# Optimization experiments

Hardware: AMD Instinct MI355X
Metric: run time of the kernel (lower is better)

The kernel has to match this reference:

```python
import jax, jax.numpy as jnp
import numpy as np

N_TOKENS, MODEL_DIM, NUM_EXPERTS = 65536, 1024, 64
CAPACITY_FACTOR = 1.0


def setup_inputs() -> dict:
    key = jax.random.key(0)
    k1, k2 = jax.random.split(key)
    x = jax.random.normal(k1, (N_TOKENS, MODEL_DIM), dtype=jnp.float32)
    # gate projection weight, torch Linear stores [out_features, in_features]
    wg = jax.random.normal(k2, (NUM_EXPERTS, MODEL_DIM), dtype=jnp.float32) * (1.0 / np.sqrt(MODEL_DIM))
    return {"x": x, "wg": wg}


def reference(x, wg):
    N, E = x.shape[0], wg.shape[0]
    logits = x @ wg.T                              # [N, E]
    # training-branch capacity: capacity_factor * ceil(N / E)
    capacity = int(CAPACITY_FACTOR * ((N + E - 1) // E))
    indices1_s = jnp.argmax(logits, axis=1)        # [N] top-1 expert per token
    gates = jax.nn.softmax(logits, axis=1)         # [N, E]
    mask1 = jax.nn.one_hot(indices1_s, E, dtype=gates.dtype)  # [N, E]
    gates1_s = jnp.sum(gates * mask1, axis=1)      # [N] gate value of chosen expert
    # locations1_s[i] = number of earlier tokens routed to the same expert
    # (exclusive prefix count = inclusive cumsum - 1 at the selected column)
    locations1 = jnp.cumsum(mask1, axis=0) - 1.0   # [N, E]
    locations1_s = jnp.sum(locations1 * mask1, axis=1).astype(jnp.int32)
    # auxiliary load-balance loss (float32 branch of the original)
    me = jnp.sum(gates, axis=0)                    # [E]
    ce = jnp.sum(mask1, axis=0)                    # [E]
    l_aux = jnp.sum(me * ce) * (E / (N * N))
    return (l_aux, indices1_s.astype(jnp.int32), capacity, locations1_s, gates1_s, E)
```

## Files before the change

kernel.cpp:

```cpp
#include <hip/hip_runtime.h>

#define NT 65536
#define MD 1024
#define NE 64
#define TB 128
#define NGATE (NT / TB)

typedef short bf16x8 __attribute__((ext_vector_type(8)));
typedef float f32x4  __attribute__((ext_vector_type(4)));

__device__ __forceinline__ void split1(float f, ushort& h, ushort& m, ushort& lo) {
    unsigned u  = __float_as_uint(f);
    unsigned hb = u & 0xFFFF0000u;
    float    r1 = f - __uint_as_float(hb);
    unsigned mb = __float_as_uint(r1) & 0xFFFF0000u;
    float    r2 = r1 - __uint_as_float(mb);
    h  = (ushort)(hb >> 16);
    m  = (ushort)(mb >> 16);
    lo = (ushort)(__float_as_uint(r2) >> 16);
}

__device__ __forceinline__ void split8(const float4 a, const float4 b,
                                       bf16x8& h, bf16x8& m, bf16x8& lo) {
    float f[8] = {a.x, a.y, a.z, a.w, b.x, b.y, b.z, b.w};
#pragma unroll
    for (int j = 0; j < 8; ++j) {
        ushort hh, mm, ll;
        split1(f[j], hh, mm, ll);
        h[j] = (short)hh; m[j] = (short)mm; lo[j] = (short)ll;
    }
}

__global__ __launch_bounds__(256) void prep_kernel(
    const float* __restrict__ wg, ushort* __restrict__ wgp,
    float* __restrict__ me)
{
    const int idx = blockIdx.x * 256 + threadIdx.x;
    if (blockIdx.x == 0 && threadIdx.x < NE) me[threadIdx.x] = 0.f;
    const int l  = idx & 63;
    const int nt = (idx >> 6) & 3;
    const int c  = idx >> 8;
    const int e  = nt * 16 + (l & 15);
    const int k0 = c * 32 + (l >> 4) * 8;
    const float* src = wg + (size_t)e * MD + k0;
    float4 a = *(const float4*)(src);
    float4 b = *(const float4*)(src + 4);
    bf16x8 h, m, lo;
    split8(a, b, h, m, lo);
    *(bf16x8*)(wgp + (size_t)idx * 8)          = h;
    *(bf16x8*)(wgp + 65536 + (size_t)idx * 8)  = m;
    *(bf16x8*)(wgp + 131072 + (size_t)idx * 8) = lo;
}

#define MFMA6(accv, xh, xm, xl, wh, wm, wl)                                        \
    accv = __builtin_amdgcn_mfma_f32_16x16x32_bf16(xh, wh, accv, 0, 0, 0);         \
    accv = __builtin_amdgcn_mfma_f32_16x16x32_bf16(xh, wm, accv, 0, 0, 0);         \
    accv = __builtin_amdgcn_mfma_f32_16x16x32_bf16(xm, wh, accv, 0, 0, 0);         \
    accv = __builtin_amdgcn_mfma_f32_16x16x32_bf16(xm, wm, accv, 0, 0, 0);         \
    accv = __builtin_amdgcn_mfma_f32_16x16x32_bf16(xh, wl, accv, 0, 0, 0);         \
    accv = __builtin_amdgcn_mfma_f32_16x16x32_bf16(xl, wh, accv, 0, 0, 0);

__global__ __launch_bounds__(512, 4) void gate_kernel(
    const float* __restrict__ x, const ushort* __restrict__ wgp,
    float* __restrict__ out, unsigned* __restrict__ packed_ws,
    int* __restrict__ hist_ws, float* __restrict__ me)
{
    __shared__ __align__(16) float uni[12288];
    __shared__ float inv[TB];
    ushort* bsm = (ushort*)uni;
    float*  lt  = uni;

    const int tid = threadIdx.x;
    const int wv  = tid >> 6;
    const int l   = tid & 63;
    const int g   = wv & 3;
    const int h   = wv >> 2;
    const int lr  = l & 15;
    const int lg  = l >> 4;

    const float* xa0 = x + (size_t)(blockIdx.x * TB + g * 32 + lr) * MD
                         + h * 512 + lg * 8;
    const float* xa1 = xa0 + 16 * MD;

    const int id0 = wv * 3;
    const int h0 = id0 / 12,       f0 = id0 % 12;
    const int h1 = (id0 + 1) / 12, f1 = (id0 + 1) % 12;
    const int h2 = (id0 + 2) / 12, f2 = (id0 + 2) % 12;
    const ushort* gs0 = wgp + (f0 >> 2) * 65536 + ((h0 * 16) * 4 + (f0 & 3)) * 512 + l * 8;
    const ushort* gs1 = wgp + (f1 >> 2) * 65536 + ((h1 * 16) * 4 + (f1 & 3)) * 512 + l * 8;
    const ushort* gs2 = wgp + (f2 >> 2) * 65536 + ((h2 * 16) * 4 + (f2 & 3)) * 512 + l * 8;

    f32x4 acc[2][4];
#pragma unroll
    for (int mt = 0; mt < 2; ++mt)
#pragma unroll
        for (int nt = 0; nt < 4; ++nt) acc[mt][nt] = f32x4{0.f, 0.f, 0.f, 0.f};

    {
        float4 v0 = *(const float4*)(gs0);
        float4 v1 = *(const float4*)(gs1);
        float4 v2 = *(const float4*)(gs2);
        *(float4*)(bsm + ((0 * 2 + h0) * 12 + f0) * 512 + l * 8) = v0;
        *(float4*)(bsm + ((0 * 2 + h1) * 12 + f1) * 512 + l * 8) = v1;
        *(float4*)(bsm + ((0 * 2 + h2) * 12 + f2) * 512 + l * 8) = v2;
    }

    float4 a00 = *(const float4*)(xa0);
    float4 a01 = *(const float4*)(xa0 + 4);
    float4 a10 = *(const float4*)(xa1);
    float4 a11 = *(const float4*)(xa1 + 4);
    __syncthreads();

    for (int s = 0; s < 16; ++s) {
        const int p = s & 1;
        float4 sv0, sv1, sv2;
        if (s < 15) {
            sv0 = *(const float4*)(gs0 + (s + 1) * 2048);
            sv1 = *(const float4*)(gs1 + (s + 1) * 2048);
            sv2 = *(const float4*)(gs2 + (s + 1) * 2048);
        }
        bf16x8 ah0, am0, al0, ah1, am1, al1;
        split8(a00, a01, ah0, am0, al0);
        split8(a10, a11, ah1, am1, al1);
        if (s < 15) {
            const float* xn0 = xa0 + (s + 1) * 32;
            const float* xn1 = xa1 + (s + 1) * 32;
            a00 = *(const float4*)(xn0);
            a01 = *(const float4*)(xn0 + 4);
            a10 = *(const float4*)(xn1);
            a11 = *(const float4*)(xn1 + 4);
        }
        const ushort* pb = bsm + (p * 2 + h) * 6144 + l * 8;
#pragma unroll
        for (int nt = 0; nt < 4; ++nt) {
            bf16x8 bh = *(const bf16x8*)(pb + (0 + nt) * 512);
            bf16x8 bm = *(const bf16x8*)(pb + (4 + nt) * 512);
            bf16x8 bl = *(const bf16x8*)(pb + (8 + nt) * 512);
            MFMA6(acc[0][nt], ah0, am0, al0, bh, bm, bl);
            MFMA6(acc[1][nt], ah1, am1, al1, bh, bm, bl);
        }
        if (s < 15) {
            const int q = p ^ 1;
            *(float4*)(bsm + ((q * 2 + h0) * 12 + f0) * 512 + l * 8) = sv0;
            *(float4*)(bsm + ((q * 2 + h1) * 12 + f1) * 512 + l * 8) = sv1;
            *(float4*)(bsm + ((q * 2 + h2) * 12 + f2) * 512 + l * 8) = sv2;
        }
        __syncthreads();
    }

    if (h == 0) {
#pragma unroll
        for (int mt = 0; mt < 2; ++mt)
#pragma unroll
            for (int nt = 0; nt < 4; ++nt)
#pragma unroll
                for (int r = 0; r < 4; ++r)
                    lt[(g * 32 + mt * 16 + lg * 4 + r) * 65 + nt * 16 + lr] =
                        acc[mt][nt][r];
    }
    __syncthreads();
    if (h == 1) {
#pragma unroll
        for (int mt = 0; mt < 2; ++mt)
#pragma unroll
            for (int nt = 0; nt < 4; ++nt)
#pragma unroll
                for (int r = 0; r < 4; ++r)
                    lt[(g * 32 + mt * 16 + lg * 4 + r) * 65 + nt * 16 + lr] +=
                        acc[mt][nt][r];
    }
    __syncthreads();

    if (tid < 128) {
        const int grp = tid >> 6;
        const int t   = tid & 63;
        float* row = &lt[(grp * 64 + t) * 65];
        float mx = -1e30f; int am = 0;
        for (int e = 0; e < NE; ++e) {
            float v = row[e];
            if (v > mx) { mx = v; am = e; }
        }
        float sum = 0.f;
        for (int e = 0; e < NE; ++e) {
            float ev = __expf(row[e] - mx);
            row[e] = ev;
            sum += ev;
        }
        float gv = 1.0f / sum;
        const int gt = blockIdx.x * TB + grp * 64 + t;
        out[1 + gt] = (float)am;
        out[2 + 2 * NT + gt] = gv;
        inv[grp * 64 + t] = gv;

        const unsigned long long below = (1ull << t) - 1ull;
        int rank = 0, mycnt = 0;
        for (int e = 0; e < NE; ++e) {
            unsigned long long msk = __ballot(am == e);
            if (t == e)  mycnt = (int)__popcll(msk);
            if (am == e) rank  = (int)__popcll(msk & below);
        }
        packed_ws[gt] = (unsigned)am | ((unsigned)rank << 8);
        hist_ws[(blockIdx.x * 2 + grp) * NE + t] = mycnt;
    }
    __syncthreads();

    if (tid < 128) {
        const int grp = tid >> 6;
        const int e   = tid & 63;
        const float* base = &lt[grp * 64 * 65];
        const float* iv   = &inv[grp * 64];
        float s = 0.f;
        for (int t = 0; t < 64; ++t) s += base[t * 65 + e] * iv[t];
        atomicAdd(&me[e], s);
    }
}

__global__ __launch_bounds__(256) void scan_kernel(
    int* __restrict__ hist_ws, float* __restrict__ ce)
{
    const int e = blockIdx.x;
    const int tid = threadIdx.x;
    const int lane = tid & 63, wave = tid >> 6;
    __shared__ int wtot[4];

    int h[4];
#pragma unroll
    for (int j = 0; j < 4; ++j) h[j] = hist_ws[(tid * 4 + j) * NE + e];
    int s = h[0] + h[1] + h[2] + h[3];

    int scan = s;
#pragma unroll
    for (int d = 1; d < 64; d <<= 1) {
        int o = __shfl_up(scan, d, 64);
        if (lane >= d) scan += o;
    }
    if (lane == 63) wtot[wave] = scan;
    __syncthreads();
    int wpre = 0;
#pragma unroll
    for (int w = 0; w < 4; ++w)
        if (w < wave) wpre += wtot[w];

    int run = wpre + scan - s;
#pragma unroll
    for (int j = 0; j < 4; ++j) {
        hist_ws[(tid * 4 + j) * NE + e] = run;
        run += h[j];
    }
    if (tid == 255) ce[e] = (float)run;
}

__global__ __launch_bounds__(256) void emit_kernel(
    const unsigned* __restrict__ packed_ws, const int* __restrict__ offs_ws,
    const float* __restrict__ me, const float* __restrict__ ce,
    float* __restrict__ out)
{
    const int i = blockIdx.x * 256 + threadIdx.x;
    const unsigned p = packed_ws[i];
    const int am = (int)(p & 63u);
    const int rank = (int)(p >> 8);
    const int b = i >> 6;
    out[2 + NT + i] = (float)(offs_ws[b * NE + am] + rank);

    if (blockIdx.x == 0 && threadIdx.x < 64) {
        float v = me[threadIdx.x] * ce[threadIdx.x];
#pragma unroll
        for (int d = 32; d > 0; d >>= 1) v += __shfl_down(v, d, 64);
        if (threadIdx.x == 0) {
            out[0] = v * (float)((double)NE / ((double)NT * (double)NT));
            out[1 + NT] = 1024.0f;
            out[2 + 3 * NT] = 64.0f;
        }
    }
}

extern "C" void kernel_launch(void* const* d_in, const int* in_sizes, int n_in,
                              void* d_out, int out_size, void* d_ws, size_t ws_size,
                              hipStream_t stream)
{
    const float* x  = (const float*)d_in[0];
    const float* wg = (const float*)d_in[1];
    float* out = (float*)d_out;

    unsigned* packed_ws = (unsigned*)d_ws;
    int*      hist_ws   = (int*)((char*)d_ws + 262144);
    float*    me        = (float*)((char*)d_ws + 524288);
    float*    ce        = (float*)((char*)d_ws + 524544);
    ushort*   wgp       = (ushort*)((char*)d_ws + 524800);

    prep_kernel<<<32, 256, 0, stream>>>(wg, wgp, me);
    gate_kernel<<<NGATE, 512, 0, stream>>>(x, wgp, out, packed_ws, hist_ws, me);
    scan_kernel<<<NE, 256, 0, stream>>>(hist_ws, ce);
    emit_kernel<<<NT / 256, 256, 0, stream>>>(packed_ws, hist_ws, me, ce, out);
}
```

Before: 382.8 us.

## Parallelize gate epilogue across all threads and replace me atomics with partials

The softmax/argmax epilogue now uses all 512 threads, four per token with shuffle reductions, instead of 128 threads each looping over 64 experts. The ballot-based rank/histogram loop is split across 8 waves, each handling 16 experts, and the column sum for me is split across 8 thread groups. Global atomicAdd on me is replaced by per-block partials that the scan kernel reduces, which also removes the zeroing in prep. This is meant to shorten the serial tail of each gate block and avoid atomic contention, at the cost of extra shared memory and an extra reduction pass in scan.

```diff
diff --git a/kernel.cpp b/kernel.cpp
--- a/kernel.cpp
+++ b/kernel.cpp
@@ -32,11 +32,9 @@
 }
 
 __global__ __launch_bounds__(256) void prep_kernel(
-    const float* __restrict__ wg, ushort* __restrict__ wgp,
-    float* __restrict__ me)
+    const float* __restrict__ wg, ushort* __restrict__ wgp)
 {
     const int idx = blockIdx.x * 256 + threadIdx.x;
-    if (blockIdx.x == 0 && threadIdx.x < NE) me[threadIdx.x] = 0.f;
     const int l  = idx & 63;
     const int nt = (idx >> 6) & 3;
     const int c  = idx >> 8;
@@ -63,10 +61,12 @@
 __global__ __launch_bounds__(512, 4) void gate_kernel(
     const float* __restrict__ x, const ushort* __restrict__ wgp,
     float* __restrict__ out, unsigned* __restrict__ packed_ws,
-    int* __restrict__ hist_ws, float* __restrict__ me)
+    int* __restrict__ hist_ws, float* __restrict__ me_part)
 {
     __shared__ __align__(16) float uni[12288];
     __shared__ float inv[TB];
+    __shared__ int   amL[TB];
+    __shared__ float sme[8][NE];
     ushort* bsm = (ushort*)uni;
     float*  lt  = uni;
 
@@ -171,62 +171,100 @@
     }
     __syncthreads();
 
-    if (tid < 128) {
-        const int grp = tid >> 6;
-        const int t   = tid & 63;
-        float* row = &lt[(grp * 64 + t) * 65];
+    {
+        const int t = tid >> 2;
+        const int q = tid & 3;
+        float* row = &lt[t * 65 + q * 16];
         float mx = -1e30f; int am = 0;
-        for (int e = 0; e < NE; ++e) {
-            float v = row[e];
-            if (v > mx) { mx = v; am = e; }
-        }
-        float sum = 0.f;
-        for (int e = 0; e < NE; ++e) {
-            float ev = __expf(row[e] - mx);
-            row[e] = ev;
-            sum += ev;
-        }
-        float gv = 1.0f / sum;
+#pragma unroll
+        for (int j = 0; j < 16; ++j) {
+            float v = row[j];
+            if (v > mx) { mx = v; am = q * 16 + j; }
+        }
+#pragma unroll
+        for (int d = 1; d < 4; d <<= 1) {
+            float om = __shfl_xor(mx, d, 64);
+            int   oa = __shfl_xor(am, d, 64);
+            if (om > mx || (om == mx && oa < am)) { mx = om; am = oa; }
+        }
+        float s = 0.f;
+#pragma unroll
+        for (int j = 0; j < 16; ++j) {
+            float ev = __expf(row[j] - mx);
+            row[j] = ev;
+            s += ev;
+        }
+#pragma unroll
+        for (int d = 1; d < 4; d <<= 1) s += __shfl_xor(s, d, 64);
+        if (q == 0) {
+            float gv = 1.0f / s;
+            const int gt = blockIdx.x * TB + t;
+            out[1 + gt] = (float)am;
+            out[2 + 2 * NT + gt] = gv;
+            inv[t] = gv;
+            amL[t] = am;
+        }
+    }
+    __syncthreads();
+
+    {
+        const int grp = wv >> 2;
+        const int e0  = (wv & 3) * 16;
+        const int t   = l;
+        const int amv = amL[grp * 64 + t];
+        const unsigned long long below = (1ull << t) - 1ull;
         const int gt = blockIdx.x * TB + grp * 64 + t;
-        out[1 + gt] = (float)am;
-        out[2 + 2 * NT + gt] = gv;
-        inv[grp * 64 + t] = gv;
-
-        const unsigned long long below = (1ull << t) - 1ull;
-        int rank = 0, mycnt = 0;
-        for (int e = 0; e < NE; ++e) {
-            unsigned long long msk = __ballot(am == e);
-            if (t == e)  mycnt = (int)__popcll(msk);
-            if (am == e) rank  = (int)__popcll(msk & below);
-        }
-        packed_ws[gt] = (unsigned)am | ((unsigned)rank << 8);
-        hist_ws[(blockIdx.x * 2 + grp) * NE + t] = mycnt;
-    }
-    __syncthreads();
-
-    if (tid < 128) {
-        const int grp = tid >> 6;
-        const int e   = tid & 63;
-        const float* base = &lt[grp * 64 * 65];
-        const float* iv   = &inv[grp * 64];
+#pragma unroll
+        for (int j = 0; j < 16; ++j) {
+            const int e = e0 + j;
+            unsigned long long msk = __ballot(amv == e);
+            if (t == e)
+                hist_ws[(blockIdx.x * 2 + grp) * NE + e] = (int)__popcll(msk);
+            if (amv == e)
+                packed_ws[gt] = (unsigned)amv | ((unsigned)__popcll(msk & below) << 8);
+        }
+    }
+
+    {
+        const int e  = tid & 63;
+        const int q8 = tid >> 6;
         float s = 0.f;
-        for (int t = 0; t < 64; ++t) s += base[t * 65 + e] * iv[t];
-        atomicAdd(&me[e], s);
+#pragma unroll
+        for (int j = 0; j < 16; ++j) {
+            const int t = q8 * 16 + j;
+            s += lt[t * 65 + e] * inv[t];
+        }
+        sme[q8][e] = s;
+    }
+    __syncthreads();
+    if (tid < NE) {
+        float s = 0.f;
+#pragma unroll
+        for (int q8 = 0; q8 < 8; ++q8) s += sme[q8][tid];
+        me_part[blockIdx.x * NE + tid] = s;
     }
 }
 
 __global__ __launch_bounds__(256) void scan_kernel(
-    int* __restrict__ hist_ws, float* __restrict__ ce)
+    int* __restrict__ hist_ws, const float* __restrict__ me_part,
+    float* __restrict__ me, float* __restrict__ ce)
 {
     const int e = blockIdx.x;
     const int tid = threadIdx.x;
     const int lane = tid & 63, wave = tid >> 6;
     __shared__ int wtot[4];
+    __shared__ float wsum[4];
 
     int h[4];
 #pragma unroll
     for (int j = 0; j < 4; ++j) h[j] = hist_ws[(tid * 4 + j) * NE + e];
     int s = h[0] + h[1] + h[2] + h[3];
+
+    float ms = me_part[(size_t)(2 * tid) * NE + e]
+             + me_part[(size_t)(2 * tid + 1) * NE + e];
+#pragma unroll
+    for (int d = 32; d > 0; d >>= 1) ms += __shfl_down(ms, d, 64);
+    if (lane == 0) wsum[wave] = ms;
 
     int scan = s;
 #pragma unroll
@@ -247,6 +285,7 @@
         hist_ws[(tid * 4 + j) * NE + e] = run;
         run += h[j];
     }
+    if (tid == 0) me[e] = wsum[0] + wsum[1] + wsum[2] + wsum[3];
     if (tid == 255) ce[e] = (float)run;
 }
 
@@ -284,12 +323,13 @@
 
     unsigned* packed_ws = (unsigned*)d_ws;
     int*      hist_ws   = (int*)((char*)d_ws + 262144);
-    float*    me        = (float*)((char*)d_ws + 524288);
-    float*    ce        = (float*)((char*)d_ws + 524544);
-    ushort*   wgp       = (ushort*)((char*)d_ws + 524800);
-
-    prep_kernel<<<32, 256, 0, stream>>>(wg, wgp, me);
-    gate_kernel<<<NGATE, 512, 0, stream>>>(x, wgp, out, packed_ws, hist_ws, me);
-    scan_kernel<<<NE, 256, 0, stream>>>(hist_ws, ce);
+    float*    me_part   = (float*)((char*)d_ws + 524288);
+    float*    me        = (float*)((char*)d_ws + 655360);
+    float*    ce        = (float*)((char*)d_ws + 655616);
+    ushort*   wgp       = (ushort*)((char*)d_ws + 655872);
+
+    prep_kernel<<<32, 256, 0, stream>>>(wg, wgp);
+    gate_kernel<<<NGATE, 512, 0, stream>>>(x, wgp, out, packed_ws, hist_ws, me_part);
+    scan_kernel<<<NE, 256, 0, stream>>>(hist_ws, me_part, me, ce);
     emit_kernel<<<NT / 256, 256, 0, stream>>>(packed_ws, hist_ws, me, ce, out);
 }
```

Result: no change. 382.4 us (-0.1%).
